# Performance work log

Measured on AMD Instinct MI355X. Metric: run time of the kernel, lower is better.

Reference implementation:

```python
import jax, jax.numpy as jnp
import numpy as np

BN_EPS = 1e-5


def _conv1d(x, w, b):
    # x: (B, C, T), w: (O, C, K), torch Conv1d with padding=K//2
    k = w.shape[-1]
    p = k // 2
    out = jax.lax.conv_general_dilated(
        x, w, window_strides=(1,), padding=[(p, p)],
        dimension_numbers=("NCH", "OIH", "NCH"))
    return out + b[None, :, None]


def setup_inputs() -> dict:
    key = jax.random.key(0)
    ks = jax.random.split(key, 16)
    B, C, T, H, NC = 32, 13, 2048, 128, 10
    d = {
        "x": jax.random.normal(ks[0], (B, C, T), jnp.float32),
        "w1": jax.random.normal(ks[1], (H, C, 10), jnp.float32) * 0.1,
        "b1": jax.random.normal(ks[2], (H,), jnp.float32) * 0.1,
        "w2": jax.random.normal(ks[3], (H, C, 20), jnp.float32) * 0.1,
        "b2": jax.random.normal(ks[4], (H,), jnp.float32) * 0.1,
        "w3": jax.random.normal(ks[5], (H, C, 30), jnp.float32) * 0.1,
        "b3": jax.random.normal(ks[6], (H,), jnp.float32) * 0.1,
        "w4": jax.random.normal(ks[7], (H, C, 40), jnp.float32) * 0.1,
        "b4": jax.random.normal(ks[8], (H,), jnp.float32) * 0.1,
        "bn_gamma": jax.random.uniform(ks[9], (4 * H,), jnp.float32, 0.5, 1.5),
        "bn_beta": jax.random.normal(ks[10], (4 * H,), jnp.float32) * 0.1,
        "bn_mean": jnp.zeros((4 * H,), jnp.float32),
        "bn_var": jnp.ones((4 * H,), jnp.float32),
        "logreg_w": jax.random.normal(ks[11], (NC, 4 * H), jnp.float32) * 0.05,
        "logreg_b": jax.random.normal(ks[12], (NC,), jnp.float32) * 0.1,
        "dec_w": jax.random.normal(ks[13], (1, 4 * H), jnp.float32) * 0.05,
        "dec_b": jax.random.normal(ks[14], (1,), jnp.float32) * 0.1,
    }
    return d


def reference(x, w1, b1, w2, b2, w3, b3, w4, b4,
              bn_gamma, bn_beta, bn_mean, bn_var,
              logreg_w, logreg_b, dec_w, dec_b):
    # --- multi-scale shapelet conv + per-prefix cumulative max pooling ---
    feats = []
    for w, b in ((w1, b1), (w2, b2), (w3, b3), (w4, b4)):
        f = _conv1d(x, w, b)                      # (B, H, T+1) (even kernels)
        # original loop: for t in 1..T_out-1 take max over f[:, :, :t]
        # == running (cumulative) max, dropping the last prefix
        cm = jax.lax.cummax(f, axis=2)[:, :, :-1]  # (B, H, T)
        feats.append(jnp.transpose(cm, (0, 2, 1)))  # (B, T, H)
    features = jnp.concatenate(feats, axis=-1)      # (B, T, 4H)

    # --- BatchNorm1d over feature channels (eval mode), dropout = identity ---
    inv = jax.lax.rsqrt(bn_var + BN_EPS)
    features = (features - bn_mean) * (inv * bn_gamma) + bn_beta

    # --- classification head and halting head ---
    logits = jnp.einsum("btf,cf->btc", features, logreg_w) + logreg_b  # (B,T,NC)
    deltas = jnp.einsum("btf,of->bto", features, dec_w) + dec_b        # (B,T,1)
    deltas = jax.nn.softmax(deltas[..., 0], axis=1)                    # (B,T)

    # --- attention budget: pt_t = delta_t * budget_{t-1}; budget decays ---
    B = deltas.shape[0]
    q = 1.0 - deltas                                # (B, T)
    cp = jnp.cumprod(q[:, 1:], axis=1)              # prod_{s=1..t} q_s
    budget = jnp.concatenate([jnp.ones((B, 1), deltas.dtype), cp], axis=1)
    pts_loop = deltas[:, 1:] * budget[:, :-1]       # (B, T-1)
    pts = jnp.concatenate([pts_loop, budget[:, -1:]], axis=1)  # (B, T)

    probs = jax.nn.softmax(logits, axis=-1)  # temperature = 1
    return probs, pts
```

## Files before the change

### kernel.cpp

```cpp
#include <hip/hip_runtime.h>
#include <math.h>

#define NEG_INF (-3.402823466e38f)

typedef float f32x4 __attribute__((ext_vector_type(4)));
typedef short bf16x8 __attribute__((ext_vector_type(8)));
typedef unsigned int u32x4 __attribute__((ext_vector_type(4)));

__device__ __forceinline__ unsigned short f2bf(float f) {
    unsigned int u = __float_as_uint(f);
    unsigned int r = (u + 0x7FFFu + ((u >> 16) & 1u)) >> 16;
    return (unsigned short)r;
}
__device__ __forceinline__ float bf2f(unsigned short s) {
    return __uint_as_float(((unsigned int)s) << 16);
}
__device__ __forceinline__ unsigned int pack2(float a, float b) {
    return (unsigned int)f2bf(a) | ((unsigned int)f2bf(b) << 16);
}
__device__ __forceinline__ int swz(int a) { return a ^ (((a >> 5) & 7) << 4); }

__global__ __launch_bounds__(512) void prep_kernel(
    const float* __restrict__ x,
    const float* __restrict__ w1, const float* __restrict__ w2,
    const float* __restrict__ w3, const float* __restrict__ w4,
    const float* __restrict__ bn_gamma, const float* __restrict__ bn_beta,
    const float* __restrict__ bn_mean, const float* __restrict__ bn_var,
    const float* __restrict__ lw, const float* __restrict__ lb,
    const float* __restrict__ dw, const float* __restrict__ db,
    unsigned short* __restrict__ xT, unsigned short* __restrict__ Bfrag,
    unsigned short* __restrict__ hfrag, float* __restrict__ bfo,
    float* __restrict__ dbfo)
{
    int bid = blockIdx.x;
    int tid = threadIdx.x;
    if (bid < 136) {
        int idx = bid * 512 + tid;
        int b = idx / 2176, r = idx - b * 2176;
        int t = r - 20;
        unsigned short row[16];
#pragma unroll
        for (int c = 0; c < 16; ++c) {
            float v = (c < 13 && t >= 0 && t < 2048) ? x[((size_t)(b * 13 + c)) * 2048 + t] : 0.f;
            row[c] = f2bf(v);
        }
        u32x4* dst = (u32x4*)(xT + (size_t)idx * 16);
        u32x4 v0, v1;
        v0.x = row[0] | ((unsigned)row[1] << 16);  v0.y = row[2] | ((unsigned)row[3] << 16);
        v0.z = row[4] | ((unsigned)row[5] << 16);  v0.w = row[6] | ((unsigned)row[7] << 16);
        v1.x = row[8] | ((unsigned)row[9] << 16);  v1.y = row[10] | ((unsigned)row[11] << 16);
        v1.z = row[12] | ((unsigned)row[13] << 16); v1.w = row[14] | ((unsigned)row[15] << 16);
        dst[0] = v0; dst[1] = v1;
    } else if (bid < 186) {
        int idx = (bid - 136) * 512 + tid;
        int lane = idx & 63, frag = idx >> 6;
        int rel, Kc; const float* w;
        if (frag < 40)       { rel = frag;       w = w1; Kc = 10; }
        else if (frag < 120) { rel = frag - 40;  w = w2; Kc = 20; }
        else if (frag < 240) { rel = frag - 120; w = w3; Kc = 30; }
        else                 { rel = frag - 240; w = w4; Kc = 40; }
        int kh = Kc / 2;
        int ht = rel / kh;
        int k0 = rel - ht * kh;
        int h = ht * 16 + (lane & 15);
        int dk = lane >> 5;
        int cbase = 8 * ((lane >> 4) & 1);
        int k = 2 * k0 + dk;
        unsigned short e[8];
#pragma unroll
        for (int j = 0; j < 8; ++j) {
            int c = cbase + j;
            float v = (c < 13) ? w[((size_t)h * 13 + c) * Kc + k] : 0.f;
            e[j] = f2bf(v);
        }
        u32x4 pk;
        pk.x = e[0] | ((unsigned)e[1] << 16); pk.y = e[2] | ((unsigned)e[3] << 16);
        pk.z = e[4] | ((unsigned)e[5] << 16); pk.w = e[6] | ((unsigned)e[7] << 16);
        *(u32x4*)(Bfrag + (size_t)frag * 512 + lane * 8) = pk;
    } else if (bid == 186) {
        __shared__ float sh[512];
        int j = tid;
        float s = rsqrtf(bn_var[j] + 1e-5f) * bn_gamma[j];
        float shift = bn_beta[j] - bn_mean[j] * s;
        sh[j] = shift;
        __syncthreads();
        if (j < 10) {
            float acc = lb[j];
            for (int q = 0; q < 512; ++q) acc += sh[q] * lw[j * 512 + q];
            bfo[j] = acc;
        } else if (j == 10) {
            float acc = db[0];
            for (int q = 0; q < 512; ++q) acc += sh[q] * dw[q];
            dbfo[0] = acc;
        }
    } else {
        int idx = (bid - 187) * 512 + tid;
        int lane = idx & 63, frag = idx >> 6;
        int n = lane & 15;
        unsigned short e[8];
#pragma unroll
        for (int jj = 0; jj < 8; ++jj) {
            int k = frag * 32 + 8 * (lane >> 4) + jj;
            float s = rsqrtf(bn_var[k] + 1e-5f) * bn_gamma[k];
            float v = (n < 10) ? lw[n * 512 + k] * s : (n == 10) ? dw[k] * s : 0.f;
            e[jj] = f2bf(v);
        }
        u32x4 pk;
        pk.x = e[0] | ((unsigned)e[1] << 16); pk.y = e[2] | ((unsigned)e[3] << 16);
        pk.z = e[4] | ((unsigned)e[5] << 16); pk.w = e[6] | ((unsigned)e[7] << 16);
        *(u32x4*)(hfrag + (size_t)frag * 512 + lane * 8) = pk;
    }
}

__global__ __launch_bounds__(256, 4) void conv_mfma(
    const unsigned short* __restrict__ xT, const unsigned short* __restrict__ Bfrag,
    const float* __restrict__ b1, const float* __restrict__ b2,
    const float* __restrict__ b3, const float* __restrict__ b4,
    unsigned short* __restrict__ feat, unsigned short* __restrict__ totals)
{
    __shared__ __align__(16) unsigned short lds[2688 + 2 * 32 * 132];
    unsigned short* xs = lds;
    unsigned int* stg32 = (unsigned int*)(lds + 2688);
    const int tid = threadIdx.x;
    const int tq = blockIdx.x & 15;
    const int scale = (blockIdx.x >> 4) & 3;
    const int b = blockIdx.x >> 6;
    const int kh_tab[4] = {5, 10, 15, 20};
    const int so_tab[4] = {0, 40, 120, 240};
    const int KH = kh_tab[scale];
    const int P = 5 * (scale + 1);
    const float* bias = (scale == 0) ? b1 : (scale == 1) ? b2 : (scale == 2) ? b3 : b4;

    const unsigned short* src = xT + ((size_t)b * 2176 + tq * 128) * 16;
#pragma unroll
    for (int it = 0; it < 2; ++it) {
        int c = it * 256 + tid;
        if (c < 336) {
            u32x4 v = *(const u32x4*)(src + c * 8);
            *(u32x4*)((char*)xs + swz(c * 16)) = v;
        }
    }
    __syncthreads();

    const int lane = tid & 63;
    const int wave = tid >> 6;
    const int hgrp = wave & 1;
    const int twq = wave >> 1;
    const int l15 = lane & 15;
    const int g4 = lane >> 4;

    const unsigned short* bfr = Bfrag + ((size_t)(so_tab[scale] + hgrp * 4 * KH)) * 512 + lane * 8;
    float bv[4];
#pragma unroll
    for (int ht = 0; ht < 4; ++ht) bv[ht] = bias[hgrp * 64 + ht * 16 + l15];

    int abase = ((20 - P) + twq * 64 + l15 + (lane >> 5)) * 32 + ((lane >> 4) & 1) * 16;

    f32x4 acc[4][4];
#pragma unroll
    for (int ht = 0; ht < 4; ++ht)
#pragma unroll
        for (int tt = 0; tt < 4; ++tt)
            acc[ht][tt] = (f32x4){bv[ht], bv[ht], bv[ht], bv[ht]};

#pragma unroll 1
    for (int k0 = 0; k0 < KH; ++k0) {
        bf16x8 B[4], A[4];
#pragma unroll
        for (int ht = 0; ht < 4; ++ht)
            B[ht] = *(const bf16x8*)(bfr + (size_t)(ht * KH + k0) * 512);
#pragma unroll
        for (int tt = 0; tt < 4; ++tt)
            A[tt] = *(const bf16x8*)((const char*)xs + swz(abase + tt * 512 + k0 * 64));
#pragma unroll
        for (int ht = 0; ht < 4; ++ht)
#pragma unroll
            for (int tt = 0; tt < 4; ++tt)
                acc[ht][tt] = __builtin_amdgcn_mfma_f32_16x16x32_bf16(A[tt], B[ht], acc[ht][tt], 0, 0, 0);
    }

    float carry[4] = {NEG_INF, NEG_INF, NEG_INF, NEG_INF};
    const int rq = tq * 2 + twq;
#pragma unroll
    for (int tt = 0; tt < 4; ++tt) {
#pragma unroll
        for (int ht = 0; ht < 4; ++ht) {
            f32x4 v = acc[ht][tt];
            float s0 = v.x;
            float s1 = fmaxf(v.y, s0);
            float s2 = fmaxf(v.z, s1);
            float s3 = fmaxf(v.w, s2);
            float inc = s3;
            float o = __shfl_up(inc, 16); if (lane >= 16) inc = fmaxf(inc, o);
            o = __shfl_up(inc, 32);       if (lane >= 32) inc = fmaxf(inc, o);
            float pre = __shfl_up(inc, 16);
            float base = (lane >= 16) ? fmaxf(carry[ht], pre) : carry[ht];
            s0 = fmaxf(s0, base); s1 = fmaxf(s1, base);
            s2 = fmaxf(s2, base); s3 = fmaxf(s3, base);
            float tot = __shfl(inc, l15 + 48);
            carry[ht] = fmaxf(carry[ht], tot);
            acc[ht][tt] = (f32x4){s0, s1, s2, s3};
        }
    }
    if (lane < 16) {
#pragma unroll
        for (int ht = 0; ht < 4; ++ht) {
            int j = scale * 128 + hgrp * 64 + ht * 16 + l15;
            totals[((size_t)b * 32 + rq) * 512 + j] = f2bf(carry[ht]);
        }
    }

#pragma unroll 1
    for (int half = 0; half < 2; ++half) {
        if (half) __syncthreads();
        if (twq == half) {
#pragma unroll
            for (int tt = 0; tt < 4; ++tt) {
#pragma unroll
                for (int ht = 0; ht < 4; ++ht) {
                    f32x4 s = acc[ht][tt];
                    int r2 = tt * 8 + 2 * g4;
                    int cc = hgrp * 64 + ht * 16 + l15;
                    stg32[r2 * 132 + cc]       = pack2(s.x, s.y);
                    stg32[(r2 + 1) * 132 + cc] = pack2(s.z, s.w);
                }
            }
        }
        __syncthreads();
        size_t grow = (size_t)b * 2048 + tq * 128 + half * 64;
#pragma unroll
        for (int i = 0; i < 2; ++i) {
            int e = i * 256 + tid;
            int r2 = e >> 4, q = e & 15;
            const unsigned int* p = stg32 + r2 * 132 + q * 8;
            u32x4 da = *(const u32x4*)(p);
            u32x4 dbb = *(const u32x4*)(p + 4);
            u32x4 ev, od;
            ev.x = (da.x & 0xffffu) | (da.y << 16);
            ev.y = (da.z & 0xffffu) | (da.w << 16);
            ev.z = (dbb.x & 0xffffu) | (dbb.y << 16);
            ev.w = (dbb.z & 0xffffu) | (dbb.w << 16);
            od.x = (da.x >> 16) | (da.y & 0xffff0000u);
            od.y = (da.z >> 16) | (da.w & 0xffff0000u);
            od.z = (dbb.x >> 16) | (dbb.y & 0xffff0000u);
            od.w = (dbb.z >> 16) | (dbb.w & 0xffff0000u);
            size_t base = (grow + 2 * r2) * 512 + scale * 128 + q * 8;
            *(u32x4*)(feat + base)       = ev;
            *(u32x4*)(feat + base + 512) = od;
        }
    }
}

__global__ __launch_bounds__(256) void head_kernel(
    const unsigned short* __restrict__ feat, const unsigned short* __restrict__ totals,
    const unsigned short* __restrict__ hfrag, const float* __restrict__ bfo,
    const float* __restrict__ dbfo, float* __restrict__ probs,
    float* __restrict__ delta_raw)
{
    __shared__ float pfs[512];
    int b = blockIdx.x >> 5;
    int tc = blockIdx.x & 31;
    int tid = threadIdx.x;
    int lane = tid & 63;
    int wave = tid >> 6;

    for (int j = tid; j < 512; j += 256) {
        float run = NEG_INF;
        for (int qq = 0; qq < tc; ++qq)
            run = fmaxf(run, bf2f(totals[((size_t)b * 32 + qq) * 512 + j]));
        pfs[j] = run;
    }
    __syncthreads();

    bf16x8 Bf[16];
#pragma unroll
    for (int k0 = 0; k0 < 16; ++k0)
        Bf[k0] = *(const bf16x8*)(hfrag + (size_t)k0 * 512 + lane * 8);

    const int n = lane & 15;
    const int g4 = lane >> 4;
    const int tb = tc * 64 + wave * 16;
    const unsigned short* fb = feat + ((size_t)b * 2048 + tb + n) * 512 + 8 * g4;

    float biasv = (n < 10) ? bfo[n] : (n == 10) ? dbfo[0] : 0.f;
    f32x4 acc = (f32x4){biasv, biasv, biasv, biasv};

#pragma unroll
    for (int k0 = 0; k0 < 16; ++k0) {
        bf16x8 a = *(const bf16x8*)(fb + k0 * 32);
        const float* pp = pfs + k0 * 32 + 8 * g4;
        union { unsigned int u[4]; bf16x8 v; } aw;
#pragma unroll
        for (int i = 0; i < 4; ++i) {
            float lo = fmaxf(bf2f((unsigned short)a[2 * i]),     pp[2 * i]);
            float hi = fmaxf(bf2f((unsigned short)a[2 * i + 1]), pp[2 * i + 1]);
            aw.u[i] = (__float_as_uint(lo) >> 16) | (__float_as_uint(hi) & 0xFFFF0000u);
        }
        acc = __builtin_amdgcn_mfma_f32_16x16x32_bf16(aw.v, Bf[k0], acc, 0, 0, 0);
    }

#pragma unroll
    for (int r = 0; r < 4; ++r) {
        float v = acc[r];
        float vm = (n < 10) ? v : NEG_INF;
#pragma unroll
        for (int off = 1; off < 16; off <<= 1)
            vm = fmaxf(vm, __shfl_xor(vm, off, 16));
        float e = (n < 10) ? __expf(v - vm) : 0.f;
        float s = e;
#pragma unroll
        for (int off = 1; off < 16; off <<= 1)
            s += __shfl_xor(s, off, 16);
        int t = tb + g4 * 4 + r;
        if (n < 10) probs[((size_t)b * 2048 + t) * 10 + n] = e / s;
        if (n == 10) delta_raw[b * 2048 + t] = v;
    }
}

__global__ __launch_bounds__(256) void budget_kernel(
    const float* __restrict__ delta_raw, float* __restrict__ pts)
{
    __shared__ float ds[2048];
    __shared__ float red[8];
    int b = blockIdx.x;
    int tid = threadIdx.x;
    int lane = tid & 63, wid = tid >> 6;
    const float* row = delta_raw + b * 2048;
    int base = tid * 8;
    float d[8];
#pragma unroll
    for (int i = 0; i < 8; ++i) d[i] = row[base + i];
    float m = d[0];
#pragma unroll
    for (int i = 1; i < 8; ++i) m = fmaxf(m, d[i]);
#pragma unroll
    for (int off = 1; off < 64; off <<= 1) m = fmaxf(m, __shfl_xor(m, off));
    if (lane == 0) red[wid] = m;
    __syncthreads();
    m = fmaxf(fmaxf(red[0], red[1]), fmaxf(red[2], red[3]));
    float s = 0.f;
#pragma unroll
    for (int i = 0; i < 8; ++i) { d[i] = __expf(d[i] - m); s += d[i]; }
#pragma unroll
    for (int off = 1; off < 64; off <<= 1) s += __shfl_xor(s, off);
    if (lane == 0) red[4 + wid] = s;
    __syncthreads();
    float inv = 1.f / (red[4] + red[5] + red[6] + red[7]);
    float g[8], p = 1.f;
#pragma unroll
    for (int i = 0; i < 8; ++i) {
        d[i] *= inv;
        ds[base + i] = d[i];
        float gv = (base + i == 0) ? 1.f : (1.f - d[i]);
        p *= gv;
        g[i] = p;
    }
    float sp = p;
#pragma unroll
    for (int off = 1; off < 64; off <<= 1) {
        float o = __shfl_up(sp, off);
        if (lane >= off) sp *= o;
    }
    float pre_t = __shfl_up(sp, 1);
    if (lane == 0) pre_t = 1.f;
    if (lane == 63) red[wid] = sp;
    __syncthreads();
    float wpre = 1.f;
#pragma unroll
    for (int w = 0; w < 4; ++w) if (w < wid) wpre *= red[w];
    float pre = wpre * pre_t;
#pragma unroll
    for (int i = 0; i < 8; ++i) {
        int t = base + i;
        float budget = pre * g[i];
        float pt = (t < 2047) ? ds[t + 1] * budget : budget;
        pts[b * 2048 + t] = pt;
    }
}

extern "C" void kernel_launch(void* const* d_in, const int* in_sizes, int n_in,
                              void* d_out, int out_size, void* d_ws, size_t ws_size,
                              hipStream_t stream)
{
    const float* x     = (const float*)d_in[0];
    const float* w1    = (const float*)d_in[1];
    const float* b1    = (const float*)d_in[2];
    const float* w2    = (const float*)d_in[3];
    const float* b2    = (const float*)d_in[4];
    const float* w3    = (const float*)d_in[5];
    const float* b3    = (const float*)d_in[6];
    const float* w4    = (const float*)d_in[7];
    const float* b4    = (const float*)d_in[8];
    const float* gamma = (const float*)d_in[9];
    const float* beta  = (const float*)d_in[10];
    const float* mean  = (const float*)d_in[11];
    const float* var   = (const float*)d_in[12];
    const float* lw    = (const float*)d_in[13];
    const float* lb    = (const float*)d_in[14];
    const float* dw    = (const float*)d_in[15];
    const float* db    = (const float*)d_in[16];

    char* ws = (char*)d_ws;
    unsigned short* feat   = (unsigned short*)ws;
    unsigned short* xT     = (unsigned short*)(ws + 67108864);
    unsigned short* Bfrag  = (unsigned short*)(ws + 69337088);
    unsigned short* totals = (unsigned short*)(ws + 69746688);
    float* draw   = (float*)(ws + 70795264);
    unsigned short* hfrag = (unsigned short*)(ws + 71057408);
    float* bfo    = (float*)(ws + 71073792);
    float* dbfo   = (float*)(ws + 71073856);

    float* probs = (float*)d_out;
    float* pts   = probs + (size_t)32 * 2048 * 10;

    hipLaunchKernelGGL(prep_kernel, dim3(189), dim3(512), 0, stream,
                       x, w1, w2, w3, w4, gamma, beta, mean, var,
                       lw, lb, dw, db, xT, Bfrag, hfrag, bfo, dbfo);
    hipLaunchKernelGGL(conv_mfma, dim3(2048), dim3(256), 0, stream,
                       xT, Bfrag, b1, b2, b3, b4, feat, totals);
    hipLaunchKernelGGL(head_kernel, dim3(1024), dim3(256), 0, stream,
                       feat, totals, hfrag, bfo, dbfo, probs, draw);
    hipLaunchKernelGGL(budget_kernel, dim3(32), dim3(256), 0, stream, draw, pts);
}
```

Measured before the change: 89.83 us.

## Template conv on kernel size, unroll K loop, single-pass staging, coalesced x transpose

The conv kernel is templated on the per-scale kernel half-width, so the K loop can be fully unrolled and scale dispatch becomes a switch. The epilogue now writes the cumulative-max results straight into a doubled LDS staging buffer and drains all rows after one barrier, replacing the two-half pass. Occupancy drops to 2 blocks per SM. The prep kernel moves to 256-thread blocks and transposes x through shared memory so the global reads are coalesced. The larger LDS footprint and higher register use from unrolling may reduce latency hiding.

After: 90.60 us. Within noise of the previous version (+0.9%).

```diff
diff --git a/kernel.cpp b/kernel.cpp
--- a/kernel.cpp
+++ b/kernel.cpp
@@ -20,7 +20,7 @@
 }
 __device__ __forceinline__ int swz(int a) { return a ^ (((a >> 5) & 7) << 4); }
 
-__global__ __launch_bounds__(512) void prep_kernel(
+__global__ __launch_bounds__(256) void prep_kernel(
     const float* __restrict__ x,
     const float* __restrict__ w1, const float* __restrict__ w2,
     const float* __restrict__ w3, const float* __restrict__ w4,
@@ -34,25 +34,32 @@
 {
     int bid = blockIdx.x;
     int tid = threadIdx.x;
-    if (bid < 136) {
-        int idx = bid * 512 + tid;
-        int b = idx / 2176, r = idx - b * 2176;
-        int t = r - 20;
-        unsigned short row[16];
-#pragma unroll
-        for (int c = 0; c < 16; ++c) {
-            float v = (c < 13 && t >= 0 && t < 2048) ? x[((size_t)(b * 13 + c)) * 2048 + t] : 0.f;
-            row[c] = f2bf(v);
-        }
-        u32x4* dst = (u32x4*)(xT + (size_t)idx * 16);
-        u32x4 v0, v1;
-        v0.x = row[0] | ((unsigned)row[1] << 16);  v0.y = row[2] | ((unsigned)row[3] << 16);
-        v0.z = row[4] | ((unsigned)row[5] << 16);  v0.w = row[6] | ((unsigned)row[7] << 16);
-        v1.x = row[8] | ((unsigned)row[9] << 16);  v1.y = row[10] | ((unsigned)row[11] << 16);
-        v1.z = row[12] | ((unsigned)row[13] << 16); v1.w = row[14] | ((unsigned)row[15] << 16);
-        dst[0] = v0; dst[1] = v1;
-    } else if (bid < 186) {
-        int idx = (bid - 136) * 512 + tid;
+    if (bid < 288) {
+        __shared__ float xsp[13][257];
+        int b = bid / 9;
+        int chunk = bid - b * 9;
+        int r0 = chunk * 256;
+        int t = r0 - 20 + tid;
+#pragma unroll
+        for (int c = 0; c < 13; ++c)
+            xsp[c][tid] = (t >= 0 && t < 2048) ? x[((size_t)(b * 13 + c)) * 2048 + t] : 0.f;
+        __syncthreads();
+        int r = r0 + tid;
+        if (r < 2176) {
+            unsigned short row[16];
+#pragma unroll
+            for (int c = 0; c < 13; ++c) row[c] = f2bf(xsp[c][tid]);
+            row[13] = 0; row[14] = 0; row[15] = 0;
+            u32x4 v0, v1;
+            v0.x = row[0] | ((unsigned)row[1] << 16);  v0.y = row[2] | ((unsigned)row[3] << 16);
+            v0.z = row[4] | ((unsigned)row[5] << 16);  v0.w = row[6] | ((unsigned)row[7] << 16);
+            v1.x = row[8] | ((unsigned)row[9] << 16);  v1.y = row[10] | ((unsigned)row[11] << 16);
+            v1.z = row[12] | ((unsigned)row[13] << 16); v1.w = row[14] | ((unsigned)row[15] << 16);
+            u32x4* dst = (u32x4*)(xT + ((size_t)b * 2176 + r) * 16);
+            dst[0] = v0; dst[1] = v1;
+        }
+    } else if (bid < 388) {
+        int idx = (bid - 288) * 256 + tid;
         int lane = idx & 63, frag = idx >> 6;
         int rel, Kc; const float* w;
         if (frag < 40)       { rel = frag;       w = w1; Kc = 10; }
@@ -77,24 +84,24 @@
         pk.x = e[0] | ((unsigned)e[1] << 16); pk.y = e[2] | ((unsigned)e[3] << 16);
         pk.z = e[4] | ((unsigned)e[5] << 16); pk.w = e[6] | ((unsigned)e[7] << 16);
         *(u32x4*)(Bfrag + (size_t)frag * 512 + lane * 8) = pk;
-    } else if (bid == 186) {
+    } else if (bid == 388) {
         __shared__ float sh[512];
-        int j = tid;
-        float s = rsqrtf(bn_var[j] + 1e-5f) * bn_gamma[j];
-        float shift = bn_beta[j] - bn_mean[j] * s;
-        sh[j] = shift;
+        for (int j = tid; j < 512; j += 256) {
+            float s = rsqrtf(bn_var[j] + 1e-5f) * bn_gamma[j];
+            sh[j] = bn_beta[j] - bn_mean[j] * s;
+        }
         __syncthreads();
-        if (j < 10) {
-            float acc = lb[j];
-            for (int q = 0; q < 512; ++q) acc += sh[q] * lw[j * 512 + q];
-            bfo[j] = acc;
-        } else if (j == 10) {
+        if (tid < 10) {
+            float acc = lb[tid];
+            for (int q = 0; q < 512; ++q) acc += sh[q] * lw[tid * 512 + q];
+            bfo[tid] = acc;
+        } else if (tid == 10) {
             float acc = db[0];
             for (int q = 0; q < 512; ++q) acc += sh[q] * dw[q];
             dbfo[0] = acc;
         }
     } else {
-        int idx = (bid - 187) * 512 + tid;
+        int idx = (bid - 389) * 256 + tid;
         int lane = idx & 63, frag = idx >> 6;
         int n = lane & 15;
         unsigned short e[8];
@@ -112,24 +119,15 @@
     }
 }
 
-__global__ __launch_bounds__(256, 4) void conv_mfma(
+template <int KH>
+__device__ __forceinline__ void conv_core(
     const unsigned short* __restrict__ xT, const unsigned short* __restrict__ Bfrag,
-    const float* __restrict__ b1, const float* __restrict__ b2,
-    const float* __restrict__ b3, const float* __restrict__ b4,
-    unsigned short* __restrict__ feat, unsigned short* __restrict__ totals)
-{
-    __shared__ __align__(16) unsigned short lds[2688 + 2 * 32 * 132];
-    unsigned short* xs = lds;
-    unsigned int* stg32 = (unsigned int*)(lds + 2688);
+    const float* __restrict__ bias, int so,
+    unsigned short* __restrict__ feat, unsigned short* __restrict__ totals,
+    unsigned short* xs, unsigned int* stg32, int b, int scale, int tq)
+{
+    constexpr int P = KH;
     const int tid = threadIdx.x;
-    const int tq = blockIdx.x & 15;
-    const int scale = (blockIdx.x >> 4) & 3;
-    const int b = blockIdx.x >> 6;
-    const int kh_tab[4] = {5, 10, 15, 20};
-    const int so_tab[4] = {0, 40, 120, 240};
-    const int KH = kh_tab[scale];
-    const int P = 5 * (scale + 1);
-    const float* bias = (scale == 0) ? b1 : (scale == 1) ? b2 : (scale == 2) ? b3 : b4;
 
     const unsigned short* src = xT + ((size_t)b * 2176 + tq * 128) * 16;
 #pragma unroll
@@ -149,7 +147,7 @@
     const int l15 = lane & 15;
     const int g4 = lane >> 4;
 
-    const unsigned short* bfr = Bfrag + ((size_t)(so_tab[scale] + hgrp * 4 * KH)) * 512 + lane * 8;
+    const unsigned short* bfr = Bfrag + ((size_t)(so + hgrp * 4 * KH)) * 512 + lane * 8;
     float bv[4];
 #pragma unroll
     for (int ht = 0; ht < 4; ++ht) bv[ht] = bias[hgrp * 64 + ht * 16 + l15];
@@ -163,7 +161,7 @@
         for (int tt = 0; tt < 4; ++tt)
             acc[ht][tt] = (f32x4){bv[ht], bv[ht], bv[ht], bv[ht]};
 
-#pragma unroll 1
+#pragma unroll
     for (int k0 = 0; k0 < KH; ++k0) {
         bf16x8 B[4], A[4];
 #pragma unroll
@@ -181,6 +179,8 @@
 
     float carry[4] = {NEG_INF, NEG_INF, NEG_INF, NEG_INF};
     const int rq = tq * 2 + twq;
+    const int col = hgrp * 64 + l15;
+
 #pragma unroll
     for (int tt = 0; tt < 4; ++tt) {
 #pragma unroll
@@ -199,7 +199,10 @@
             s2 = fmaxf(s2, base); s3 = fmaxf(s3, base);
             float tot = __shfl(inc, l15 + 48);
             carry[ht] = fmaxf(carry[ht], tot);
-            acc[ht][tt] = (f32x4){s0, s1, s2, s3};
+            int r2 = twq * 32 + tt * 8 + 2 * g4;
+            int cc = col + ht * 16;
+            stg32[r2 * 132 + cc]       = pack2(s0, s1);
+            stg32[(r2 + 1) * 132 + cc] = pack2(s2, s3);
         }
     }
     if (lane < 16) {
@@ -209,45 +212,48 @@
             totals[((size_t)b * 32 + rq) * 512 + j] = f2bf(carry[ht]);
         }
     }
-
-#pragma unroll 1
-    for (int half = 0; half < 2; ++half) {
-        if (half) __syncthreads();
-        if (twq == half) {
-#pragma unroll
-            for (int tt = 0; tt < 4; ++tt) {
-#pragma unroll
-                for (int ht = 0; ht < 4; ++ht) {
-                    f32x4 s = acc[ht][tt];
-                    int r2 = tt * 8 + 2 * g4;
-                    int cc = hgrp * 64 + ht * 16 + l15;
-                    stg32[r2 * 132 + cc]       = pack2(s.x, s.y);
-                    stg32[(r2 + 1) * 132 + cc] = pack2(s.z, s.w);
-                }
-            }
-        }
-        __syncthreads();
-        size_t grow = (size_t)b * 2048 + tq * 128 + half * 64;
-#pragma unroll
-        for (int i = 0; i < 2; ++i) {
-            int e = i * 256 + tid;
-            int r2 = e >> 4, q = e & 15;
-            const unsigned int* p = stg32 + r2 * 132 + q * 8;
-            u32x4 da = *(const u32x4*)(p);
-            u32x4 dbb = *(const u32x4*)(p + 4);
-            u32x4 ev, od;
-            ev.x = (da.x & 0xffffu) | (da.y << 16);
-            ev.y = (da.z & 0xffffu) | (da.w << 16);
-            ev.z = (dbb.x & 0xffffu) | (dbb.y << 16);
-            ev.w = (dbb.z & 0xffffu) | (dbb.w << 16);
-            od.x = (da.x >> 16) | (da.y & 0xffff0000u);
-            od.y = (da.z >> 16) | (da.w & 0xffff0000u);
-            od.z = (dbb.x >> 16) | (dbb.y & 0xffff0000u);
-            od.w = (dbb.z >> 16) | (dbb.w & 0xffff0000u);
-            size_t base = (grow + 2 * r2) * 512 + scale * 128 + q * 8;
-            *(u32x4*)(feat + base)       = ev;
-            *(u32x4*)(feat + base + 512) = od;
-        }
+    __syncthreads();
+
+    size_t grow = (size_t)b * 2048 + tq * 128;
+#pragma unroll
+    for (int i = 0; i < 4; ++i) {
+        int e = i * 256 + tid;
+        int r2 = e >> 4, q = e & 15;
+        const unsigned int* p = stg32 + r2 * 132 + q * 8;
+        u32x4 da = *(const u32x4*)(p);
+        u32x4 dbb = *(const u32x4*)(p + 4);
+        u32x4 ev, od;
+        ev.x = (da.x & 0xffffu) | (da.y << 16);
+        ev.y = (da.z & 0xffffu) | (da.w << 16);
+        ev.z = (dbb.x & 0xffffu) | (dbb.y << 16);
+        ev.w = (dbb.z & 0xffffu) | (dbb.w << 16);
+        od.x = (da.x >> 16) | (da.y & 0xffff0000u);
+        od.y = (da.z >> 16) | (da.w & 0xffff0000u);
+        od.z = (dbb.x >> 16) | (dbb.y & 0xffff0000u);
+        od.w = (dbb.z >> 16) | (dbb.w & 0xffff0000u);
+        size_t base = (grow + 2 * r2) * 512 + scale * 128 + q * 8;
+        *(u32x4*)(feat + base)       = ev;
+        *(u32x4*)(feat + base + 512) = od;
+    }
+}
+
+__global__ __launch_bounds__(256, 2) void conv_mfma(
+    const unsigned short* __restrict__ xT, const unsigned short* __restrict__ Bfrag,
+    const float* __restrict__ b1, const float* __restrict__ b2,
+    const float* __restrict__ b3, const float* __restrict__ b4,
+    unsigned short* __restrict__ feat, unsigned short* __restrict__ totals)
+{
+    __shared__ __align__(16) unsigned short lds[2688 + 2 * 64 * 132];
+    unsigned short* xs = lds;
+    unsigned int* stg32 = (unsigned int*)(lds + 2688);
+    const int tq = blockIdx.x & 15;
+    const int scale = (blockIdx.x >> 4) & 3;
+    const int b = blockIdx.x >> 6;
+    switch (scale) {
+    case 0: conv_core<5>(xT, Bfrag, b1, 0, feat, totals, xs, stg32, b, 0, tq); break;
+    case 1: conv_core<10>(xT, Bfrag, b2, 40, feat, totals, xs, stg32, b, 1, tq); break;
+    case 2: conv_core<15>(xT, Bfrag, b3, 120, feat, totals, xs, stg32, b, 2, tq); break;
+    default: conv_core<20>(xT, Bfrag, b4, 240, feat, totals, xs, stg32, b, 3, tq); break;
     }
 }
 
@@ -413,7 +419,7 @@
     float* probs = (float*)d_out;
     float* pts   = probs + (size_t)32 * 2048 * 10;
 
-    hipLaunchKernelGGL(prep_kernel, dim3(189), dim3(512), 0, stream,
+    hipLaunchKernelGGL(prep_kernel, dim3(393), dim3(256), 0, stream,
                        x, w1, w2, w3, w4, gamma, beta, mean, var,
                        lw, lb, dw, db, xT, Bfrag, hfrag, bfo, dbfo);
     hipLaunchKernelGGL(conv_mfma, dim3(2048), dim3(256), 0, stream,
```
